# Optimization experiments

Measured on AMD Instinct MI355X. Metric: run time of the kernel, lower is better.

Reference implementation:

```python
import jax, jax.numpy as jnp
import numpy as np

B, S, D = 2, 2048, 1024
E, K, F = 8, 2, 4 * D


def setup_inputs() -> dict:
    key = jax.random.key(0)
    ks = jax.random.split(key, 5)
    sd = 1.0 / np.sqrt(D)
    sf = 1.0 / np.sqrt(F)
    x = jax.random.normal(ks[0], (B, S, D), dtype=jnp.float32)
    Wg = jax.random.uniform(ks[1], (D, E), dtype=jnp.float32, minval=-sd, maxval=sd)
    W1 = jax.random.uniform(ks[2], (E, D, F), dtype=jnp.float32, minval=-sd, maxval=sd)
    W3 = jax.random.uniform(ks[3], (D, E * F), dtype=jnp.float32, minval=-sd, maxval=sd).reshape(D, E, F).transpose(1, 0, 2)
    W2 = jax.random.uniform(ks[4], (E, F, D), dtype=jnp.float32, minval=-sf, maxval=sf)
    return {"x": x, "Wg": Wg, "W1": W1, "W2": W2, "W3": W3}


def reference(x, Wg, W1, W2, W3):
    Bx, Sx, Dx = x.shape
    xf = x.reshape(-1, Dx)  # [T, D]
    T = xf.shape[0]
    gate_logits = xf @ Wg  # [T, E]
    probs = jax.nn.softmax(gate_logits, axis=-1)
    weights, sel = jax.lax.top_k(probs, K)  # [T, K]
    weights = weights / jnp.sum(weights, axis=-1, keepdims=True)
    # scatter top-k weights into a dense [T, E] combine matrix (top-k indices are distinct)
    coef = jnp.zeros((T, W1.shape[0]), dtype=xf.dtype)
    coef = coef.at[jnp.arange(T)[:, None], sel].add(weights)
    out = jnp.zeros_like(xf)
    for e in range(W1.shape[0]):  # small fixed expert count
        h = jax.nn.silu(xf @ W1[e]) * (xf @ W3[e])  # [T, F]
        out = out + coef[:, e:e + 1] * (h @ W2[e])
    aux_loss = jnp.mean(jnp.var(gate_logits, axis=-1, ddof=1))  # torch .var() is unbiased
    return out.reshape(Bx, Sx, Dx), aux_loss
```

## Files before the change

### kernel.cpp

```cpp
#include <hip/hip_runtime.h>

typedef __bf16 bf16x8 __attribute__((ext_vector_type(8)));
typedef float  f32x4  __attribute__((ext_vector_type(4)));

#define TOKS 4096
#define DIM  1024
#define NEXP 8
#define NF   4096
#define CAP  4096
#define BM 128
#define BN 128
#define BK 64

typedef __attribute__((address_space(3))) unsigned int as3_u32;
typedef __attribute__((address_space(1))) unsigned int as1_u32;
__device__ __forceinline__ void gl16(const unsigned short* g, unsigned short* l) {
  __builtin_amdgcn_global_load_lds((as1_u32*)(unsigned long long)g, (as3_u32*)l, 16, 0, 0);
}

__device__ __forceinline__ unsigned short f2bf(float f) {
  unsigned int u = __float_as_uint(f);
  u += 0x7FFFu + ((u >> 16) & 1u);
  return (unsigned short)(u >> 16);
}
__device__ __forceinline__ int swzo(int major) {
  return ((major & 7) ^ ((major >> 3) & 7)) << 3;
}
__device__ __forceinline__ int swz8(int row, int chunk) {
  return (chunk ^ (row & 7)) << 3;
}

__global__ void moe_route(const float* __restrict__ x, const float* __restrict__ Wg,
                          int* __restrict__ pairCnt, int* __restrict__ pairIdx,
                          float* __restrict__ pairWgt, float* __restrict__ auxSum)
{
  int lane = threadIdx.x & 63;
  int tok  = blockIdx.x * 4 + (threadIdx.x >> 6);
  const float* xr = x + (size_t)tok * DIM;
  float acc[8];
  #pragma unroll
  for (int e = 0; e < 8; ++e) acc[e] = 0.f;
  #pragma unroll
  for (int i = 0; i < 16; ++i) {
    int d = i * 64 + lane;
    float xv = xr[d];
    const float4* wr = (const float4*)(Wg + d * 8);
    float4 wa = wr[0], wb = wr[1];
    acc[0] += xv * wa.x; acc[1] += xv * wa.y; acc[2] += xv * wa.z; acc[3] += xv * wa.w;
    acc[4] += xv * wb.x; acc[5] += xv * wb.y; acc[6] += xv * wb.z; acc[7] += xv * wb.w;
  }
  #pragma unroll
  for (int e = 0; e < 8; ++e) {
    float v = acc[e];
    #pragma unroll
    for (int off = 32; off; off >>= 1) v += __shfl_xor(v, off);
    acc[e] = v;
  }
  if (lane == 0) {
    int e1 = 0; float l1 = acc[0];
    #pragma unroll
    for (int e = 1; e < 8; ++e) if (acc[e] > l1) { l1 = acc[e]; e1 = e; }
    int e2 = -1; float l2 = -3.4e38f;
    #pragma unroll
    for (int e = 0; e < 8; ++e) if (e != e1 && acc[e] > l2) { l2 = acc[e]; e2 = e; }
    float r  = expf(l2 - l1);
    float w1 = 1.f / (1.f + r);
    float w2 = r / (1.f + r);
    int s1 = atomicAdd(&pairCnt[e1], 1);
    pairIdx[e1 * CAP + s1] = tok * 2;     pairWgt[e1 * CAP + s1] = w1;
    int s2 = atomicAdd(&pairCnt[e2], 1);
    pairIdx[e2 * CAP + s2] = tok * 2 + 1; pairWgt[e2 * CAP + s2] = w2;
    float m = 0.f;
    #pragma unroll
    for (int e = 0; e < 8; ++e) m += acc[e];
    m *= 0.125f;
    float v = 0.f;
    #pragma unroll
    for (int e = 0; e < 8; ++e) { float dd = acc[e] - m; v += dd * dd; }
    atomicAdd(auxSum, v * (1.f / 7.f));
  }
}

__global__ void moe_aux_final(const float* __restrict__ auxSum, float* __restrict__ outScalar) {
  *outScalar = auxSum[0] * (1.f / (float)TOKS);
}

__global__ __launch_bounds__(256) void cvt_x(const float* __restrict__ in,
                                             unsigned short* __restrict__ o)
{
  int i = (blockIdx.x * 256 + threadIdx.x) * 16;
  const float4* s = (const float4*)(in + i);
  float4 a = s[0], b = s[1], c = s[2], d = s[3];
  union { unsigned short u[8]; uint4 q; } p0, p1;
  p0.u[0]=f2bf(a.x); p0.u[1]=f2bf(a.y); p0.u[2]=f2bf(a.z); p0.u[3]=f2bf(a.w);
  p0.u[4]=f2bf(b.x); p0.u[5]=f2bf(b.y); p0.u[6]=f2bf(b.z); p0.u[7]=f2bf(b.w);
  p1.u[0]=f2bf(c.x); p1.u[1]=f2bf(c.y); p1.u[2]=f2bf(c.z); p1.u[3]=f2bf(c.w);
  p1.u[4]=f2bf(d.x); p1.u[5]=f2bf(d.y); p1.u[6]=f2bf(d.z); p1.u[7]=f2bf(d.w);
  *(uint4*)(o + i)     = p0.q;
  *(uint4*)(o + i + 8) = p1.q;
}

__global__ __launch_bounds__(256) void cvt_transpose(
    const float* __restrict__ in, unsigned short* __restrict__ outp, int R, int C)
{
  __shared__ unsigned short tile[64 * 72];
  int e  = blockIdx.z;
  int r0 = blockIdx.x * 64, c0 = blockIdx.y * 64;
  const float*    ine  = in   + (size_t)e * R * C;
  unsigned short* oute = outp + (size_t)e * R * C;
  int t = threadIdx.x;
  int r = t >> 2, cs = (t & 3) * 16;
  const float4* src = (const float4*)(ine + (size_t)(r0 + r) * C + c0 + cs);
  #pragma unroll
  for (int j = 0; j < 4; ++j) {
    float4 v = src[j];
    tile[(cs + j * 4 + 0) * 72 + r] = f2bf(v.x);
    tile[(cs + j * 4 + 1) * 72 + r] = f2bf(v.y);
    tile[(cs + j * 4 + 2) * 72 + r] = f2bf(v.z);
    tile[(cs + j * 4 + 3) * 72 + r] = f2bf(v.w);
  }
  __syncthreads();
  int c = t >> 2, rs = (t & 3) * 16;
  uint4 o0 = *(const uint4*)&tile[c * 72 + rs];
  uint4 o1 = *(const uint4*)&tile[c * 72 + rs + 8];
  unsigned short* dst = oute + (size_t)(c0 + c) * R + r0 + rs;
  *(uint4*)dst       = o0;
  *(uint4*)(dst + 8) = o1;
}

__global__ __launch_bounds__(512) void moe_ffn1_g(
    const unsigned short* __restrict__ xbf, const unsigned short* __restrict__ W1T,
    const unsigned short* __restrict__ W3T,
    const int* __restrict__ pairCnt, const int* __restrict__ pairIdx,
    unsigned short* __restrict__ hbuf)
{
  int bid = blockIdx.x;
  int m_t = (bid >> 3) & 31;
  int n_t = (bid & 7) | (((bid >> 8) & 3) << 3);
  int e   = bid >> 10;
  int cnt = pairCnt[e];
  int m0  = m_t * BM;
  if (m0 >= cnt) return;
  int n0  = n_t * BN;
  __shared__ __attribute__((aligned(16))) unsigned short As[BM * BK];
  __shared__ __attribute__((aligned(16))) unsigned short B1s[BN * BK];
  __shared__ __attribute__((aligned(16))) unsigned short B3s[BN * BK];
  __shared__ int rowPid[BM];
  int tid = threadIdx.x, lane = tid & 63, wid = tid >> 6;
  if (tid < BM) {
    int gi = m0 + tid;
    rowPid[tid] = (gi < cnt) ? pairIdx[e * CAP + gi] : -1;
  }
  const unsigned short* W1e = W1T + (size_t)e * NF * DIM + (size_t)n0 * DIM;
  const unsigned short* W3e = W3T + (size_t)e * NF * DIM + (size_t)n0 * DIM;
  f32x4 zero = {0.f, 0.f, 0.f, 0.f};
  f32x4 acc1[2][4], acc2[2][4];
  #pragma unroll
  for (int mi = 0; mi < 2; ++mi)
    #pragma unroll
    for (int ni = 0; ni < 4; ++ni) { acc1[mi][ni] = zero; acc2[mi][ni] = zero; }
  int wm = (wid >> 1) * 32, wn = (wid & 1) * 64;
  __syncthreads();

  int r0a = wid * 16 + (lane >> 3), r1a = r0a + 8;
  int p0 = rowPid[r0a], p1 = rowPid[r1a];
  size_t tk0 = (size_t)((p0 >= 0) ? (p0 >> 1) : 0);
  size_t tk1 = (size_t)((p1 >= 0) ? (p1 >> 1) : 0);
  int ch0 = ((lane & 7) ^ (r0a & 7)) * 8;
  int ch1 = ((lane & 7) ^ (r1a & 7)) * 8;
  const unsigned short* gA0  = xbf + tk0 * DIM + ch0;
  const unsigned short* gA1  = xbf + tk1 * DIM + ch1;
  const unsigned short* gB10 = W1e + (size_t)r0a * DIM + ch0;
  const unsigned short* gB11 = W1e + (size_t)r1a * DIM + ch1;
  const unsigned short* gB30 = W3e + (size_t)r0a * DIM + ch0;
  const unsigned short* gB31 = W3e + (size_t)r1a * DIM + ch1;
  unsigned short* lA0  = &As [(wid * 16) * BK];
  unsigned short* lA1  = &As [(wid * 16 + 8) * BK];
  unsigned short* lB10 = &B1s[(wid * 16) * BK];
  unsigned short* lB11 = &B1s[(wid * 16 + 8) * BK];
  unsigned short* lB30 = &B3s[(wid * 16) * BK];
  unsigned short* lB31 = &B3s[(wid * 16 + 8) * BK];

  for (int kt = 0; kt < DIM; kt += BK) {
    gl16(gA0 + kt, lA0);  gl16(gA1 + kt, lA1);
    gl16(gB10 + kt, lB10); gl16(gB11 + kt, lB11);
    gl16(gB30 + kt, lB30); gl16(gB31 + kt, lB31);
    __syncthreads();
    #pragma unroll
    for (int ks = 0; ks < 2; ++ks) {
      int kc = ks * 4 + (lane >> 4);
      bf16x8 af[2];
      #pragma unroll
      for (int mi = 0; mi < 2; ++mi) {
        int row = wm + mi * 16 + (lane & 15);
        af[mi] = *(const bf16x8*)(&As[row * BK + swz8(row, kc)]);
      }
      #pragma unroll
      for (int ni = 0; ni < 4; ++ni) {
        int f = wn + ni * 16 + (lane & 15);
        bf16x8 b1 = *(const bf16x8*)(&B1s[f * BK + swz8(f, kc)]);
        bf16x8 b3 = *(const bf16x8*)(&B3s[f * BK + swz8(f, kc)]);
        #pragma unroll
        for (int mi = 0; mi < 2; ++mi) {
          acc1[mi][ni] = __builtin_amdgcn_mfma_f32_16x16x32_bf16(af[mi], b1, acc1[mi][ni], 0, 0, 0);
          acc2[mi][ni] = __builtin_amdgcn_mfma_f32_16x16x32_bf16(af[mi], b3, acc2[mi][ni], 0, 0, 0);
        }
      }
    }
    __syncthreads();
  }
  #pragma unroll
  for (int mi = 0; mi < 2; ++mi) {
    #pragma unroll
    for (int r = 0; r < 4; ++r) {
      int row = wm + mi * 16 + ((lane >> 4) << 2) + r;
      int pid = rowPid[row];
      if (pid < 0) continue;
      size_t hb = (size_t)pid * NF + n0 + wn + (lane & 15);
      #pragma unroll
      for (int ni = 0; ni < 4; ++ni) {
        float a = acc1[mi][ni][r];
        float g = acc2[mi][ni][r];
        float s = 1.f / (1.f + __expf(-a));
        hbuf[hb + ni * 16] = f2bf(a * s * g);
      }
    }
  }
}

__global__ __launch_bounds__(512) void moe_ffn2_g(
    const unsigned short* __restrict__ hbuf, const unsigned short* __restrict__ W2T,
    const int* __restrict__ pairCnt, const int* __restrict__ pairIdx,
    const float* __restrict__ pairWgt, float* __restrict__ out)
{
  int bid = blockIdx.x;
  int n_t = bid & 7;
  int m_t = (bid >> 3) & 31;
  int e   = bid >> 8;
  int cnt = pairCnt[e];
  int m0  = m_t * BM;
  if (m0 >= cnt) return;
  int n0  = n_t * BN;
  __shared__ __attribute__((aligned(16))) unsigned short As[BM * BK];
  __shared__ __attribute__((aligned(16))) unsigned short Bs[BN * BK];
  __shared__ int   rowPid[BM];
  __shared__ float rowW[BM];
  int tid = threadIdx.x, lane = tid & 63, wid = tid >> 6;
  if (tid < BM) {
    int gi = m0 + tid;
    if (gi < cnt) { rowPid[tid] = pairIdx[e * CAP + gi]; rowW[tid] = pairWgt[e * CAP + gi]; }
    else          { rowPid[tid] = -1;                    rowW[tid] = 0.f; }
  }
  const unsigned short* W2e = W2T + (size_t)e * DIM * NF + (size_t)n0 * NF;
  f32x4 zero = {0.f, 0.f, 0.f, 0.f};
  f32x4 acc[2][4];
  #pragma unroll
  for (int mi = 0; mi < 2; ++mi)
    #pragma unroll
    for (int ni = 0; ni < 4; ++ni) acc[mi][ni] = zero;
  int wm = (wid >> 1) * 32, wn = (wid & 1) * 64;
  __syncthreads();

  int r0a = wid * 16 + (lane >> 3), r1a = r0a + 8;
  int p0 = rowPid[r0a], p1 = rowPid[r1a];
  size_t h0 = (size_t)((p0 >= 0) ? p0 : 0);
  size_t h1 = (size_t)((p1 >= 0) ? p1 : 0);
  int ch0 = ((lane & 7) ^ (r0a & 7)) * 8;
  int ch1 = ((lane & 7) ^ (r1a & 7)) * 8;
  const unsigned short* gA0 = hbuf + h0 * NF + ch0;
  const unsigned short* gA1 = hbuf + h1 * NF + ch1;
  const unsigned short* gB0 = W2e + (size_t)r0a * NF + ch0;
  const unsigned short* gB1 = W2e + (size_t)r1a * NF + ch1;
  unsigned short* lA0 = &As[(wid * 16) * BK];
  unsigned short* lA1 = &As[(wid * 16 + 8) * BK];
  unsigned short* lB0 = &Bs[(wid * 16) * BK];
  unsigned short* lB1 = &Bs[(wid * 16 + 8) * BK];

  for (int kt = 0; kt < NF; kt += BK) {
    gl16(gA0 + kt, lA0); gl16(gA1 + kt, lA1);
    gl16(gB0 + kt, lB0); gl16(gB1 + kt, lB1);
    __syncthreads();
    #pragma unroll
    for (int ks = 0; ks < 2; ++ks) {
      int kc = ks * 4 + (lane >> 4);
      bf16x8 af[2];
      #pragma unroll
      for (int mi = 0; mi < 2; ++mi) {
        int row = wm + mi * 16 + (lane & 15);
        af[mi] = *(const bf16x8*)(&As[row * BK + swz8(row, kc)]);
      }
      #pragma unroll
      for (int ni = 0; ni < 4; ++ni) {
        int dc = wn + ni * 16 + (lane & 15);
        bf16x8 b = *(const bf16x8*)(&Bs[dc * BK + swz8(dc, kc)]);
        #pragma unroll
        for (int mi = 0; mi < 2; ++mi)
          acc[mi][ni] = __builtin_amdgcn_mfma_f32_16x16x32_bf16(af[mi], b, acc[mi][ni], 0, 0, 0);
      }
    }
    __syncthreads();
  }
  #pragma unroll
  for (int mi = 0; mi < 2; ++mi) {
    #pragma unroll
    for (int r = 0; r < 4; ++r) {
      int row = wm + mi * 16 + ((lane >> 4) << 2) + r;
      int pid = rowPid[row];
      if (pid < 0) continue;
      float w = rowW[row];
      float* op = out + (size_t)(pid >> 1) * DIM + n0 + wn + (lane & 15);
      #pragma unroll
      for (int ni = 0; ni < 4; ++ni)
        atomicAdd(op + ni * 16, w * acc[mi][ni][r]);
    }
  }
}

__global__ __launch_bounds__(512) void moe_ffn1(
    const float* __restrict__ x, const float* __restrict__ W1, const float* __restrict__ W3,
    const int* __restrict__ pairCnt, const int* __restrict__ pairIdx,
    unsigned short* __restrict__ hbuf)
{
  int e   = blockIdx.z;
  int cnt = pairCnt[e];
  int m0  = blockIdx.x * BM;
  if (m0 >= cnt) return;
  int n0  = blockIdx.y * BN;
  __shared__ __attribute__((aligned(16))) unsigned short As[BM * BK];
  __shared__ __attribute__((aligned(16))) unsigned short B1s[BN * BK];
  __shared__ __attribute__((aligned(16))) unsigned short B3s[BN * BK];
  __shared__ int rowPid[BM];
  int tid = threadIdx.x;
  if (tid < BM) {
    int gi = m0 + tid;
    rowPid[tid] = (gi < cnt) ? pairIdx[e * CAP + gi] : -1;
  }
  const float* W1e = W1 + (size_t)e * DIM * NF;
  const float* W3e = W3 + (size_t)e * DIM * NF;
  f32x4 zero = {0.f, 0.f, 0.f, 0.f};
  f32x4 acc1[2][4], acc2[2][4];
  #pragma unroll
  for (int mi = 0; mi < 2; ++mi)
    #pragma unroll
    for (int ni = 0; ni < 4; ++ni) { acc1[mi][ni] = zero; acc2[mi][ni] = zero; }
  int lane = tid & 63, wid = tid >> 6;
  int wm = (wid >> 1) * 32, wn = (wid & 1) * 64;

  for (int kt = 0; kt < DIM; kt += BK) {
    __syncthreads();
    #pragma unroll
    for (int it = 0; it < 4; ++it) {
      int row = it * 32 + (tid >> 4);
      int dq  = tid & 15;
      int pid = rowPid[row];
      int tk  = (pid >= 0) ? (pid >> 1) : 0;
      float4 v = *(const float4*)(x + (size_t)tk * DIM + kt + dq * 4);
      ushort4 b; b.x = f2bf(v.x); b.y = f2bf(v.y); b.z = f2bf(v.z); b.w = f2bf(v.w);
      *(ushort4*)(&As[row * BK + ((dq * 4) ^ swzo(row))]) = b;
    }
    #pragma unroll
    for (int it = 0; it < 4; ++it) {
      int d  = it * 16 + (tid >> 5);
      int fq = tid & 31;
      size_t go = (size_t)(kt + d) * NF + n0 + fq * 4;
      float4 v1 = *(const float4*)(W1e + go);
      float4 v3 = *(const float4*)(W3e + go);
      const float* p1 = (const float*)&v1;
      const float* p3 = (const float*)&v3;
      #pragma unroll
      for (int i = 0; i < 4; ++i) {
        int f   = fq * 4 + i;
        int idx = f * BK + (d ^ swzo(f));
        B1s[idx] = f2bf(p1[i]);
        B3s[idx] = f2bf(p3[i]);
      }
    }
    __syncthreads();
    #pragma unroll
    for (int ks = 0; ks < 2; ++ks) {
      int kb = ks * 32 + ((lane >> 4) << 3);
      bf16x8 af[2];
      #pragma unroll
      for (int mi = 0; mi < 2; ++mi) {
        int row = wm + mi * 16 + (lane & 15);
        af[mi] = *(const bf16x8*)(&As[row * BK + (kb ^ swzo(row))]);
      }
      #pragma unroll
      for (int ni = 0; ni < 4; ++ni) {
        int f = wn + ni * 16 + (lane & 15);
        bf16x8 b1 = *(const bf16x8*)(&B1s[f * BK + (kb ^ swzo(f))]);
        bf16x8 b3 = *(const bf16x8*)(&B3s[f * BK + (kb ^ swzo(f))]);
        #pragma unroll
        for (int mi = 0; mi < 2; ++mi) {
          acc1[mi][ni] = __builtin_amdgcn_mfma_f32_16x16x32_bf16(af[mi], b1, acc1[mi][ni], 0, 0, 0);
          acc2[mi][ni] = __builtin_amdgcn_mfma_f32_16x16x32_bf16(af[mi], b3, acc2[mi][ni], 0, 0, 0);
        }
      }
    }
  }
  #pragma unroll
  for (int mi = 0; mi < 2; ++mi) {
    #pragma unroll
    for (int r = 0; r < 4; ++r) {
      int row = wm + mi * 16 + ((lane >> 4) << 2) + r;
      int pid = rowPid[row];
      if (pid < 0) continue;
      size_t hb = (size_t)pid * NF + n0 + wn + (lane & 15);
      #pragma unroll
      for (int ni = 0; ni < 4; ++ni) {
        float a = acc1[mi][ni][r];
        float g = acc2[mi][ni][r];
        float s = 1.f / (1.f + __expf(-a));
        hbuf[hb + ni * 16] = f2bf(a * s * g);
      }
    }
  }
}

__global__ __launch_bounds__(512) void moe_ffn2(
    const unsigned short* __restrict__ hbuf, const float* __restrict__ W2,
    const int* __restrict__ pairCnt, const int* __restrict__ pairIdx,
    const float* __restrict__ pairWgt, float* __restrict__ out)
{
  int e   = blockIdx.z;
  int cnt = pairCnt[e];
  int m0  = blockIdx.x * BM;
  if (m0 >= cnt) return;
  int n0  = blockIdx.y * BN;
  __shared__ __attribute__((aligned(16))) unsigned short As[BM * BK];
  __shared__ __attribute__((aligned(16))) unsigned short Bs[BN * BK];
  __shared__ int   rowPid[BM];
  __shared__ float rowW[BM];
  int tid = threadIdx.x;
  if (tid < BM) {
    int gi = m0 + tid;
    if (gi < cnt) { rowPid[tid] = pairIdx[e * CAP + gi]; rowW[tid] = pairWgt[e * CAP + gi]; }
    else          { rowPid[tid] = -1;                    rowW[tid] = 0.f; }
  }
  const float* W2e = W2 + (size_t)e * NF * DIM;
  f32x4 zero = {0.f, 0.f, 0.f, 0.f};
  f32x4 acc[2][4];
  #pragma unroll
  for (int mi = 0; mi < 2; ++mi)
    #pragma unroll
    for (int ni = 0; ni < 4; ++ni) acc[mi][ni] = zero;
  int lane = tid & 63, wid = tid >> 6;
  int wm = (wid >> 1) * 32, wn = (wid & 1) * 64;

  for (int kt = 0; kt < NF; kt += BK) {
    __syncthreads();
    #pragma unroll
    for (int it = 0; it < 2; ++it) {
      int row = it * 64 + (tid >> 3);
      int c8  = tid & 7;
      int pid = rowPid[row];
      int pr  = (pid >= 0) ? pid : 0;
      uint4 v = *(const uint4*)(hbuf + (size_t)pr * NF + kt + c8 * 8);
      *(uint4*)(&As[row * BK + ((c8 * 8) ^ swzo(row))]) = v;
    }
    #pragma unroll
    for (int it = 0; it < 4; ++it) {
      int fk = it * 16 + (tid >> 5);
      int dq = tid & 31;
      float4 v = *(const float4*)(W2e + (size_t)(kt + fk) * DIM + n0 + dq * 4);
      const float* p = (const float*)&v;
      #pragma unroll
      for (int i = 0; i < 4; ++i) {
        int dc = dq * 4 + i;
        Bs[dc * BK + (fk ^ swzo(dc))] = f2bf(p[i]);
      }
    }
    __syncthreads();
    #pragma unroll
    for (int ks = 0; ks < 2; ++ks) {
      int kb = ks * 32 + ((lane >> 4) << 3);
      bf16x8 af[2];
      #pragma unroll
      for (int mi = 0; mi < 2; ++mi) {
        int row = wm + mi * 16 + (lane & 15);
        af[mi] = *(const bf16x8*)(&As[row * BK + (kb ^ swzo(row))]);
      }
      #pragma unroll
      for (int ni = 0; ni < 4; ++ni) {
        int dc = wn + ni * 16 + (lane & 15);
        bf16x8 b = *(const bf16x8*)(&Bs[dc * BK + (kb ^ swzo(dc))]);
        #pragma unroll
        for (int mi = 0; mi < 2; ++mi)
          acc[mi][ni] = __builtin_amdgcn_mfma_f32_16x16x32_bf16(af[mi], b, acc[mi][ni], 0, 0, 0);
      }
    }
  }
  #pragma unroll
  for (int mi = 0; mi < 2; ++mi) {
    #pragma unroll
    for (int r = 0; r < 4; ++r) {
      int row = wm + mi * 16 + ((lane >> 4) << 2) + r;
      int pid = rowPid[row];
      if (pid < 0) continue;
      float w = rowW[row];
      float* op = out + (size_t)(pid >> 1) * DIM + n0 + wn + (lane & 15);
      #pragma unroll
      for (int ni = 0; ni < 4; ++ni)
        atomicAdd(op + ni * 16, w * acc[mi][ni][r]);
    }
  }
}

extern "C" void kernel_launch(void* const* d_in, const int* in_sizes, int n_in,
                              void* d_out, int out_size, void* d_ws, size_t ws_size,
                              hipStream_t stream)
{
  const float* x  = (const float*)d_in[0];
  const float* Wg = (const float*)d_in[1];
  const float* W1 = (const float*)d_in[2];
  const float* W2 = (const float*)d_in[3];
  const float* W3 = (const float*)d_in[4];
  float* out = (float*)d_out;
  char*  ws  = (char*)d_ws;
  int*   pairCnt = (int*)ws;
  float* auxSum  = (float*)(ws + 64);
  int*   pairIdx = (int*)(ws + 4096);
  float* pairWgt = (float*)(ws + 262144);
  unsigned short* xbf  = (unsigned short*)(ws + ((size_t)1 << 20));
  unsigned short* hbuf = (unsigned short*)(ws + ((size_t)9 << 20));
  unsigned short* W1T  = (unsigned short*)(ws + ((size_t)73 << 20));
  unsigned short* W3T  = (unsigned short*)(ws + ((size_t)137 << 20));
  unsigned short* W2T  = (unsigned short*)(ws + ((size_t)201 << 20));
  const size_t WS_NEED = (size_t)265 << 20;

  hipMemsetAsync(ws, 0, 128, stream);
  hipMemsetAsync(d_out, 0, (size_t)out_size * sizeof(float), stream);
  moe_route<<<TOKS / 4, 256, 0, stream>>>(x, Wg, pairCnt, pairIdx, pairWgt, auxSum);
  moe_aux_final<<<1, 1, 0, stream>>>(auxSum, out + (out_size - 1));

  if (ws_size >= WS_NEED) {
    cvt_x<<<TOKS * DIM / (256 * 16), 256, 0, stream>>>(x, xbf);
    cvt_transpose<<<dim3(DIM / 64, NF / 64, NEXP), 256, 0, stream>>>(W1, W1T, DIM, NF);
    cvt_transpose<<<dim3(DIM / 64, NF / 64, NEXP), 256, 0, stream>>>(W3, W3T, DIM, NF);
    cvt_transpose<<<dim3(NF / 64, DIM / 64, NEXP), 256, 0, stream>>>(W2, W2T, NF, DIM);
    moe_ffn1_g<<<(TOKS / BM) * (NF / BN) * NEXP, 512, 0, stream>>>(xbf, W1T, W3T, pairCnt, pairIdx, hbuf);
    moe_ffn2_g<<<(TOKS / BM) * (DIM / BN) * NEXP, 512, 0, stream>>>(hbuf, W2T, pairCnt, pairIdx, pairWgt, out);
  } else {
    moe_ffn1<<<dim3(TOKS / BM, NF / BN, NEXP), 512, 0, stream>>>(x, W1, W3, pairCnt, pairIdx, hbuf);
    moe_ffn2<<<dim3(TOKS / BM, DIM / BN, NEXP), 512, 0, stream>>>(hbuf, W2, pairCnt, pairIdx, pairWgt, out);
  }
}
```

Before: 545.1 us.

## Double-buffer LDS tiles in MoE FFN GEMMs and load A fragments directly to registers

Both grouped expert GEMMs now keep two LDS buffers and issue the next K-tile's global-to-LDS loads before computing on the current one, using an explicit vmcnt drain plus barrier. This overlaps memory latency with MFMA work instead of serialising load, sync and compute. In FFN1 the gathered token rows of x are loaded straight into registers per lane rather than staged through LDS, which frees shared memory for the second weight buffer. The trade-offs are more LDS per block, a full vmcnt(0) drain at every barrier, and uncoalesced register gathers for the A operand.

```diff
diff --git a/kernel.cpp b/kernel.cpp
--- a/kernel.cpp
+++ b/kernel.cpp
@@ -17,6 +17,10 @@
 __device__ __forceinline__ void gl16(const unsigned short* g, unsigned short* l) {
   __builtin_amdgcn_global_load_lds((as1_u32*)(unsigned long long)g, (as3_u32*)l, 16, 0, 0);
 }
+#define DRAIN_BAR() do { \
+  asm volatile("s_waitcnt vmcnt(0)" ::: "memory"); \
+  __builtin_amdgcn_s_barrier(); \
+} while (0)
 
 __device__ __forceinline__ unsigned short f2bf(float f) {
   unsigned int u = __float_as_uint(f);
@@ -128,7 +132,24 @@
   *(uint4*)(dst + 8) = o1;
 }
 
-__global__ __launch_bounds__(512) void moe_ffn1_g(
+__device__ __forceinline__ void ffn1_mma(
+    const unsigned short* B1b, const unsigned short* B3b,
+    bf16x8 a0, bf16x8 a1, int kc, int wn, int lane,
+    f32x4 acc1[2][4], f32x4 acc2[2][4])
+{
+  #pragma unroll
+  for (int ni = 0; ni < 4; ++ni) {
+    int f = wn + ni * 16 + (lane & 15);
+    bf16x8 b1 = *(const bf16x8*)(&B1b[f * BK + swz8(f, kc)]);
+    bf16x8 b3 = *(const bf16x8*)(&B3b[f * BK + swz8(f, kc)]);
+    acc1[0][ni] = __builtin_amdgcn_mfma_f32_16x16x32_bf16(a0, b1, acc1[0][ni], 0, 0, 0);
+    acc2[0][ni] = __builtin_amdgcn_mfma_f32_16x16x32_bf16(a0, b3, acc2[0][ni], 0, 0, 0);
+    acc1[1][ni] = __builtin_amdgcn_mfma_f32_16x16x32_bf16(a1, b1, acc1[1][ni], 0, 0, 0);
+    acc2[1][ni] = __builtin_amdgcn_mfma_f32_16x16x32_bf16(a1, b3, acc2[1][ni], 0, 0, 0);
+  }
+}
+
+__global__ __launch_bounds__(512, 4) void moe_ffn1_p(
     const unsigned short* __restrict__ xbf, const unsigned short* __restrict__ W1T,
     const unsigned short* __restrict__ W3T,
     const int* __restrict__ pairCnt, const int* __restrict__ pairIdx,
@@ -142,9 +163,8 @@
   int m0  = m_t * BM;
   if (m0 >= cnt) return;
   int n0  = n_t * BN;
-  __shared__ __attribute__((aligned(16))) unsigned short As[BM * BK];
-  __shared__ __attribute__((aligned(16))) unsigned short B1s[BN * BK];
-  __shared__ __attribute__((aligned(16))) unsigned short B3s[BN * BK];
+  __shared__ __attribute__((aligned(16))) unsigned short B1s[2][BN * BK];
+  __shared__ __attribute__((aligned(16))) unsigned short B3s[2][BN * BK];
   __shared__ int rowPid[BM];
   int tid = threadIdx.x, lane = tid & 63, wid = tid >> 6;
   if (tid < BM) {
@@ -163,51 +183,53 @@
   __syncthreads();
 
   int r0a = wid * 16 + (lane >> 3), r1a = r0a + 8;
-  int p0 = rowPid[r0a], p1 = rowPid[r1a];
-  size_t tk0 = (size_t)((p0 >= 0) ? (p0 >> 1) : 0);
-  size_t tk1 = (size_t)((p1 >= 0) ? (p1 >> 1) : 0);
   int ch0 = ((lane & 7) ^ (r0a & 7)) * 8;
   int ch1 = ((lane & 7) ^ (r1a & 7)) * 8;
-  const unsigned short* gA0  = xbf + tk0 * DIM + ch0;
-  const unsigned short* gA1  = xbf + tk1 * DIM + ch1;
   const unsigned short* gB10 = W1e + (size_t)r0a * DIM + ch0;
   const unsigned short* gB11 = W1e + (size_t)r1a * DIM + ch1;
   const unsigned short* gB30 = W3e + (size_t)r0a * DIM + ch0;
   const unsigned short* gB31 = W3e + (size_t)r1a * DIM + ch1;
-  unsigned short* lA0  = &As [(wid * 16) * BK];
-  unsigned short* lA1  = &As [(wid * 16 + 8) * BK];
-  unsigned short* lB10 = &B1s[(wid * 16) * BK];
-  unsigned short* lB11 = &B1s[(wid * 16 + 8) * BK];
-  unsigned short* lB30 = &B3s[(wid * 16) * BK];
-  unsigned short* lB31 = &B3s[(wid * 16 + 8) * BK];
-
-  for (int kt = 0; kt < DIM; kt += BK) {
-    gl16(gA0 + kt, lA0);  gl16(gA1 + kt, lA1);
-    gl16(gB10 + kt, lB10); gl16(gB11 + kt, lB11);
-    gl16(gB30 + kt, lB30); gl16(gB31 + kt, lB31);
-    __syncthreads();
-    #pragma unroll
-    for (int ks = 0; ks < 2; ++ks) {
-      int kc = ks * 4 + (lane >> 4);
-      bf16x8 af[2];
-      #pragma unroll
-      for (int mi = 0; mi < 2; ++mi) {
-        int row = wm + mi * 16 + (lane & 15);
-        af[mi] = *(const bf16x8*)(&As[row * BK + swz8(row, kc)]);
-      }
-      #pragma unroll
-      for (int ni = 0; ni < 4; ++ni) {
-        int f = wn + ni * 16 + (lane & 15);
-        bf16x8 b1 = *(const bf16x8*)(&B1s[f * BK + swz8(f, kc)]);
-        bf16x8 b3 = *(const bf16x8*)(&B3s[f * BK + swz8(f, kc)]);
-        #pragma unroll
-        for (int mi = 0; mi < 2; ++mi) {
-          acc1[mi][ni] = __builtin_amdgcn_mfma_f32_16x16x32_bf16(af[mi], b1, acc1[mi][ni], 0, 0, 0);
-          acc2[mi][ni] = __builtin_amdgcn_mfma_f32_16x16x32_bf16(af[mi], b3, acc2[mi][ni], 0, 0, 0);
-        }
-      }
-    }
-    __syncthreads();
+  unsigned short* l1b0 = &B1s[0][(wid * 16) * BK];
+  unsigned short* l1b1 = &B1s[1][(wid * 16) * BK];
+  unsigned short* l3b0 = &B3s[0][(wid * 16) * BK];
+  unsigned short* l3b1 = &B3s[1][(wid * 16) * BK];
+
+  int pm0 = rowPid[wm + (lane & 15)];
+  int pm1 = rowPid[wm + 16 + (lane & 15)];
+  const unsigned short* pA0 = xbf + (size_t)((pm0 >= 0) ? (pm0 >> 1) : 0) * DIM + (lane >> 4) * 8;
+  const unsigned short* pA1 = xbf + (size_t)((pm1 >= 0) ? (pm1 >> 1) : 0) * DIM + (lane >> 4) * 8;
+
+  gl16(gB10, l1b0); gl16(gB11, l1b0 + 8 * BK);
+  gl16(gB30, l3b0); gl16(gB31, l3b0 + 8 * BK);
+  bf16x8 aA00 = *(const bf16x8*)(pA0);
+  bf16x8 aA01 = *(const bf16x8*)(pA0 + 32);
+  bf16x8 aA10 = *(const bf16x8*)(pA1);
+  bf16x8 aA11 = *(const bf16x8*)(pA1 + 32);
+  DRAIN_BAR();
+
+  for (int kt = 0; kt < DIM; kt += 2 * BK) {
+    int kN = kt + BK;
+    gl16(gB10 + kN, l1b1); gl16(gB11 + kN, l1b1 + 8 * BK);
+    gl16(gB30 + kN, l3b1); gl16(gB31 + kN, l3b1 + 8 * BK);
+    bf16x8 aB00 = *(const bf16x8*)(pA0 + kN);
+    bf16x8 aB01 = *(const bf16x8*)(pA0 + kN + 32);
+    bf16x8 aB10 = *(const bf16x8*)(pA1 + kN);
+    bf16x8 aB11 = *(const bf16x8*)(pA1 + kN + 32);
+    ffn1_mma(B1s[0], B3s[0], aA00, aA10, (lane >> 4),     wn, lane, acc1, acc2);
+    ffn1_mma(B1s[0], B3s[0], aA01, aA11, 4 + (lane >> 4), wn, lane, acc1, acc2);
+    DRAIN_BAR();
+    int kP = kt + 2 * BK;
+    if (kP < DIM) {
+      gl16(gB10 + kP, l1b0); gl16(gB11 + kP, l1b0 + 8 * BK);
+      gl16(gB30 + kP, l3b0); gl16(gB31 + kP, l3b0 + 8 * BK);
+      aA00 = *(const bf16x8*)(pA0 + kP);
+      aA01 = *(const bf16x8*)(pA0 + kP + 32);
+      aA10 = *(const bf16x8*)(pA1 + kP);
+      aA11 = *(const bf16x8*)(pA1 + kP + 32);
+    }
+    ffn1_mma(B1s[1], B3s[1], aB00, aB10, (lane >> 4),     wn, lane, acc1, acc2);
+    ffn1_mma(B1s[1], B3s[1], aB01, aB11, 4 + (lane >> 4), wn, lane, acc1, acc2);
+    DRAIN_BAR();
   }
   #pragma unroll
   for (int mi = 0; mi < 2; ++mi) {
@@ -228,7 +250,31 @@
   }
 }
 
-__global__ __launch_bounds__(512) void moe_ffn2_g(
+__device__ __forceinline__ void ffn2_mma(
+    const unsigned short* Ab, const unsigned short* Bb,
+    int wm, int wn, int lane, f32x4 acc[2][4])
+{
+  #pragma unroll
+  for (int ks = 0; ks < 2; ++ks) {
+    int kc = ks * 4 + (lane >> 4);
+    bf16x8 af[2];
+    #pragma unroll
+    for (int mi = 0; mi < 2; ++mi) {
+      int row = wm + mi * 16 + (lane & 15);
+      af[mi] = *(const bf16x8*)(&Ab[row * BK + swz8(row, kc)]);
+    }
+    #pragma unroll
+    for (int ni = 0; ni < 4; ++ni) {
+      int dc = wn + ni * 16 + (lane & 15);
+      bf16x8 b = *(const bf16x8*)(&Bb[dc * BK + swz8(dc, kc)]);
+      #pragma unroll
+      for (int mi = 0; mi < 2; ++mi)
+        acc[mi][ni] = __builtin_amdgcn_mfma_f32_16x16x32_bf16(af[mi], b, acc[mi][ni], 0, 0, 0);
+    }
+  }
+}
+
+__global__ __launch_bounds__(512, 4) void moe_ffn2_p(
     const unsigned short* __restrict__ hbuf, const unsigned short* __restrict__ W2T,
     const int* __restrict__ pairCnt, const int* __restrict__ pairIdx,
     const float* __restrict__ pairWgt, float* __restrict__ out)
@@ -241,8 +287,8 @@
   int m0  = m_t * BM;
   if (m0 >= cnt) return;
   int n0  = n_t * BN;
-  __shared__ __attribute__((aligned(16))) unsigned short As[BM * BK];
-  __shared__ __attribute__((aligned(16))) unsigned short Bs[BN * BK];
+  __shared__ __attribute__((aligned(16))) unsigned short As[2][BM * BK];
+  __shared__ __attribute__((aligned(16))) unsigned short Bs[2][BN * BK];
   __shared__ int   rowPid[BM];
   __shared__ float rowW[BM];
   int tid = threadIdx.x, lane = tid & 63, wid = tid >> 6;
@@ -271,34 +317,28 @@
   const unsigned short* gA1 = hbuf + h1 * NF + ch1;
   const unsigned short* gB0 = W2e + (size_t)r0a * NF + ch0;
   const unsigned short* gB1 = W2e + (size_t)r1a * NF + ch1;
-  unsigned short* lA0 = &As[(wid * 16) * BK];
-  unsigned short* lA1 = &As[(wid * 16 + 8) * BK];
-  unsigned short* lB0 = &Bs[(wid * 16) * BK];
-  unsigned short* lB1 = &Bs[(wid * 16 + 8) * BK];
-
-  for (int kt = 0; kt < NF; kt += BK) {
-    gl16(gA0 + kt, lA0); gl16(gA1 + kt, lA1);
-    gl16(gB0 + kt, lB0); gl16(gB1 + kt, lB1);
-    __syncthreads();
-    #pragma unroll
-    for (int ks = 0; ks < 2; ++ks) {
-      int kc = ks * 4 + (lane >> 4);
-      bf16x8 af[2];
-      #pragma unroll
-      for (int mi = 0; mi < 2; ++mi) {
-        int row = wm + mi * 16 + (lane & 15);
-        af[mi] = *(const bf16x8*)(&As[row * BK + swz8(row, kc)]);
-      }
-      #pragma unroll
-      for (int ni = 0; ni < 4; ++ni) {
-        int dc = wn + ni * 16 + (lane & 15);
-        bf16x8 b = *(const bf16x8*)(&Bs[dc * BK + swz8(dc, kc)]);
-        #pragma unroll
-        for (int mi = 0; mi < 2; ++mi)
-          acc[mi][ni] = __builtin_amdgcn_mfma_f32_16x16x32_bf16(af[mi], b, acc[mi][ni], 0, 0, 0);
-      }
-    }
-    __syncthreads();
+  unsigned short* lab0 = &As[0][(wid * 16) * BK];
+  unsigned short* lab1 = &As[1][(wid * 16) * BK];
+  unsigned short* lbb0 = &Bs[0][(wid * 16) * BK];
+  unsigned short* lbb1 = &Bs[1][(wid * 16) * BK];
+
+  gl16(gA0, lab0); gl16(gA1, lab0 + 8 * BK);
+  gl16(gB0, lbb0); gl16(gB1, lbb0 + 8 * BK);
+  DRAIN_BAR();
+
+  for (int kt = 0; kt < NF; kt += 2 * BK) {
+    int kN = kt + BK;
+    gl16(gA0 + kN, lab1); gl16(gA1 + kN, lab1 + 8 * BK);
+    gl16(gB0 + kN, lbb1); gl16(gB1 + kN, lbb1 + 8 * BK);
+    ffn2_mma(As[0], Bs[0], wm, wn, lane, acc);
+    DRAIN_BAR();
+    int kP = kt + 2 * BK;
+    if (kP < NF) {
+      gl16(gA0 + kP, lab0); gl16(gA1 + kP, lab0 + 8 * BK);
+      gl16(gB0 + kP, lbb0); gl16(gB1 + kP, lbb0 + 8 * BK);
+    }
+    ffn2_mma(As[1], Bs[1], wm, wn, lane, acc);
+    DRAIN_BAR();
   }
   #pragma unroll
   for (int mi = 0; mi < 2; ++mi) {
@@ -538,8 +578,8 @@
     cvt_transpose<<<dim3(DIM / 64, NF / 64, NEXP), 256, 0, stream>>>(W1, W1T, DIM, NF);
     cvt_transpose<<<dim3(DIM / 64, NF / 64, NEXP), 256, 0, stream>>>(W3, W3T, DIM, NF);
     cvt_transpose<<<dim3(NF / 64, DIM / 64, NEXP), 256, 0, stream>>>(W2, W2T, NF, DIM);
-    moe_ffn1_g<<<(TOKS / BM) * (NF / BN) * NEXP, 512, 0, stream>>>(xbf, W1T, W3T, pairCnt, pairIdx, hbuf);
-    moe_ffn2_g<<<(TOKS / BM) * (DIM / BN) * NEXP, 512, 0, stream>>>(hbuf, W2T, pairCnt, pairIdx, pairWgt, out);
+    moe_ffn1_p<<<(TOKS / BM) * (NF / BN) * NEXP, 512, 0, stream>>>(xbf, W1T, W3T, pairCnt, pairIdx, hbuf);
+    moe_ffn2_p<<<(TOKS / BM) * (DIM / BN) * NEXP, 512, 0, stream>>>(hbuf, W2T, pairCnt, pairIdx, pairWgt, out);
   } else {
     moe_ffn1<<<dim3(TOKS / BM, NF / BN, NEXP), 512, 0, stream>>>(x, W1, W3, pairCnt, pairIdx, hbuf);
     moe_ffn2<<<dim3(TOKS / BM, DIM / BN, NEXP), 512, 0, stream>>>(hbuf, W2, pairCnt, pairIdx, pairWgt, out);
```

Measured after the change: 734.0 us. 34.7% more time.

## Interleave W1/W3 into one transposed buffer and halve FFN1 accumulator tiles

Applied to the files above, without the earlier changes.

W1 and W3 are now converted and transposed together into one interleaved bf16 buffer, alternating 16-row groups of each. FFN1 loads a single B tile per K step and computes gate and up projections as adjacent column groups inside one accumulator set. This halves the per-block accumulator registers and shared memory, which should raise occupancy, and also fuses two conversion launches into one. In exchange FFN1 launches twice as many blocks, and each block reloads its A tile for only 64 output features.

```diff
diff --git a/kernel.cpp b/kernel.cpp
--- a/kernel.cpp
+++ b/kernel.cpp
@@ -128,37 +128,78 @@
   *(uint4*)(dst + 8) = o1;
 }
 
-__global__ __launch_bounds__(512) void moe_ffn1_g(
-    const unsigned short* __restrict__ xbf, const unsigned short* __restrict__ W1T,
-    const unsigned short* __restrict__ W3T,
+__global__ __launch_bounds__(256) void cvt_w13(
+    const float* __restrict__ W1, const float* __restrict__ W3,
+    unsigned short* __restrict__ outp)
+{
+  __shared__ unsigned short t1[64 * 72];
+  __shared__ unsigned short t3[64 * 72];
+  int e  = blockIdx.z;
+  int r0 = blockIdx.x * 64, c0 = blockIdx.y * 64;
+  const float* in1 = W1 + (size_t)e * DIM * NF;
+  const float* in3 = W3 + (size_t)e * DIM * NF;
+  unsigned short* oute = outp + (size_t)e * (2 * NF) * DIM;
+  int t = threadIdx.x;
+  int r = t >> 2, cs = (t & 3) * 16;
+  const float4* s1 = (const float4*)(in1 + (size_t)(r0 + r) * NF + c0 + cs);
+  const float4* s3 = (const float4*)(in3 + (size_t)(r0 + r) * NF + c0 + cs);
+  #pragma unroll
+  for (int j = 0; j < 4; ++j) {
+    float4 v1 = s1[j];
+    float4 v3 = s3[j];
+    int cb = cs + j * 4;
+    t1[(cb + 0) * 72 + r] = f2bf(v1.x);
+    t1[(cb + 1) * 72 + r] = f2bf(v1.y);
+    t1[(cb + 2) * 72 + r] = f2bf(v1.z);
+    t1[(cb + 3) * 72 + r] = f2bf(v1.w);
+    t3[(cb + 0) * 72 + r] = f2bf(v3.x);
+    t3[(cb + 1) * 72 + r] = f2bf(v3.y);
+    t3[(cb + 2) * 72 + r] = f2bf(v3.z);
+    t3[(cb + 3) * 72 + r] = f2bf(v3.w);
+  }
+  __syncthreads();
+  int c = t >> 2, rs = (t & 3) * 16;
+  int drow = c0 * 2 + (c >> 4) * 32 + (c & 15);
+  uint4 a0 = *(const uint4*)&t1[c * 72 + rs];
+  uint4 a1 = *(const uint4*)&t1[c * 72 + rs + 8];
+  uint4 b0 = *(const uint4*)&t3[c * 72 + rs];
+  uint4 b1 = *(const uint4*)&t3[c * 72 + rs + 8];
+  unsigned short* d1 = oute + (size_t)drow * DIM + r0 + rs;
+  unsigned short* d3 = d1 + (size_t)16 * DIM;
+  *(uint4*)d1       = a0;
+  *(uint4*)(d1 + 8) = a1;
+  *(uint4*)d3       = b0;
+  *(uint4*)(d3 + 8) = b1;
+}
+
+__global__ __launch_bounds__(512) void moe_ffn1_i(
+    const unsigned short* __restrict__ xbf, const unsigned short* __restrict__ W13T,
     const int* __restrict__ pairCnt, const int* __restrict__ pairIdx,
     unsigned short* __restrict__ hbuf)
 {
   int bid = blockIdx.x;
   int m_t = (bid >> 3) & 31;
-  int n_t = (bid & 7) | (((bid >> 8) & 3) << 3);
-  int e   = bid >> 10;
+  int n_t = (bid & 7) | (((bid >> 8) & 7) << 3);
+  int e   = bid >> 11;
   int cnt = pairCnt[e];
   int m0  = m_t * BM;
   if (m0 >= cnt) return;
-  int n0  = n_t * BN;
+  int n0f = n_t * 64;
   __shared__ __attribute__((aligned(16))) unsigned short As[BM * BK];
-  __shared__ __attribute__((aligned(16))) unsigned short B1s[BN * BK];
-  __shared__ __attribute__((aligned(16))) unsigned short B3s[BN * BK];
+  __shared__ __attribute__((aligned(16))) unsigned short Bs[BN * BK];
   __shared__ int rowPid[BM];
   int tid = threadIdx.x, lane = tid & 63, wid = tid >> 6;
   if (tid < BM) {
     int gi = m0 + tid;
     rowPid[tid] = (gi < cnt) ? pairIdx[e * CAP + gi] : -1;
   }
-  const unsigned short* W1e = W1T + (size_t)e * NF * DIM + (size_t)n0 * DIM;
-  const unsigned short* W3e = W3T + (size_t)e * NF * DIM + (size_t)n0 * DIM;
+  const unsigned short* W13e = W13T + (size_t)e * (2 * NF) * DIM + (size_t)n_t * 128 * DIM;
   f32x4 zero = {0.f, 0.f, 0.f, 0.f};
-  f32x4 acc1[2][4], acc2[2][4];
+  f32x4 acc[2][4];
   #pragma unroll
   for (int mi = 0; mi < 2; ++mi)
     #pragma unroll
-    for (int ni = 0; ni < 4; ++ni) { acc1[mi][ni] = zero; acc2[mi][ni] = zero; }
+    for (int ni = 0; ni < 4; ++ni) acc[mi][ni] = zero;
   int wm = (wid >> 1) * 32, wn = (wid & 1) * 64;
   __syncthreads();
 
@@ -168,23 +209,18 @@
   size_t tk1 = (size_t)((p1 >= 0) ? (p1 >> 1) : 0);
   int ch0 = ((lane & 7) ^ (r0a & 7)) * 8;
   int ch1 = ((lane & 7) ^ (r1a & 7)) * 8;
-  const unsigned short* gA0  = xbf + tk0 * DIM + ch0;
-  const unsigned short* gA1  = xbf + tk1 * DIM + ch1;
-  const unsigned short* gB10 = W1e + (size_t)r0a * DIM + ch0;
-  const unsigned short* gB11 = W1e + (size_t)r1a * DIM + ch1;
-  const unsigned short* gB30 = W3e + (size_t)r0a * DIM + ch0;
-  const unsigned short* gB31 = W3e + (size_t)r1a * DIM + ch1;
-  unsigned short* lA0  = &As [(wid * 16) * BK];
-  unsigned short* lA1  = &As [(wid * 16 + 8) * BK];
-  unsigned short* lB10 = &B1s[(wid * 16) * BK];
-  unsigned short* lB11 = &B1s[(wid * 16 + 8) * BK];
-  unsigned short* lB30 = &B3s[(wid * 16) * BK];
-  unsigned short* lB31 = &B3s[(wid * 16 + 8) * BK];
+  const unsigned short* gA0 = xbf + tk0 * DIM + ch0;
+  const unsigned short* gA1 = xbf + tk1 * DIM + ch1;
+  const unsigned short* gB0 = W13e + (size_t)r0a * DIM + ch0;
+  const unsigned short* gB1 = W13e + (size_t)r1a * DIM + ch1;
+  unsigned short* lA0 = &As[(wid * 16) * BK];
+  unsigned short* lA1 = &As[(wid * 16 + 8) * BK];
+  unsigned short* lB0 = &Bs[(wid * 16) * BK];
+  unsigned short* lB1 = &Bs[(wid * 16 + 8) * BK];
 
   for (int kt = 0; kt < DIM; kt += BK) {
-    gl16(gA0 + kt, lA0);  gl16(gA1 + kt, lA1);
-    gl16(gB10 + kt, lB10); gl16(gB11 + kt, lB11);
-    gl16(gB30 + kt, lB30); gl16(gB31 + kt, lB31);
+    gl16(gA0 + kt, lA0); gl16(gA1 + kt, lA1);
+    gl16(gB0 + kt, lB0); gl16(gB1 + kt, lB1);
     __syncthreads();
     #pragma unroll
     for (int ks = 0; ks < 2; ++ks) {
@@ -197,14 +233,11 @@
       }
       #pragma unroll
       for (int ni = 0; ni < 4; ++ni) {
-        int f = wn + ni * 16 + (lane & 15);
-        bf16x8 b1 = *(const bf16x8*)(&B1s[f * BK + swz8(f, kc)]);
-        bf16x8 b3 = *(const bf16x8*)(&B3s[f * BK + swz8(f, kc)]);
+        int br = wn + ni * 16 + (lane & 15);
+        bf16x8 b = *(const bf16x8*)(&Bs[br * BK + swz8(br, kc)]);
         #pragma unroll
-        for (int mi = 0; mi < 2; ++mi) {
-          acc1[mi][ni] = __builtin_amdgcn_mfma_f32_16x16x32_bf16(af[mi], b1, acc1[mi][ni], 0, 0, 0);
-          acc2[mi][ni] = __builtin_amdgcn_mfma_f32_16x16x32_bf16(af[mi], b3, acc2[mi][ni], 0, 0, 0);
-        }
+        for (int mi = 0; mi < 2; ++mi)
+          acc[mi][ni] = __builtin_amdgcn_mfma_f32_16x16x32_bf16(af[mi], b, acc[mi][ni], 0, 0, 0);
       }
     }
     __syncthreads();
@@ -216,13 +249,13 @@
       int row = wm + mi * 16 + ((lane >> 4) << 2) + r;
       int pid = rowPid[row];
       if (pid < 0) continue;
-      size_t hb = (size_t)pid * NF + n0 + wn + (lane & 15);
-      #pragma unroll
-      for (int ni = 0; ni < 4; ++ni) {
-        float a = acc1[mi][ni][r];
-        float g = acc2[mi][ni][r];
+      size_t hb = (size_t)pid * NF + n0f + (wn >> 1) + (lane & 15);
+      #pragma unroll
+      for (int fg = 0; fg < 2; ++fg) {
+        float a = acc[mi][fg * 2 + 0][r];
+        float g = acc[mi][fg * 2 + 1][r];
         float s = 1.f / (1.f + __expf(-a));
-        hbuf[hb + ni * 16] = f2bf(a * s * g);
+        hbuf[hb + fg * 16] = f2bf(a * s * g);
       }
     }
   }
@@ -523,8 +556,7 @@
   float* pairWgt = (float*)(ws + 262144);
   unsigned short* xbf  = (unsigned short*)(ws + ((size_t)1 << 20));
   unsigned short* hbuf = (unsigned short*)(ws + ((size_t)9 << 20));
-  unsigned short* W1T  = (unsigned short*)(ws + ((size_t)73 << 20));
-  unsigned short* W3T  = (unsigned short*)(ws + ((size_t)137 << 20));
+  unsigned short* W13T = (unsigned short*)(ws + ((size_t)73 << 20));
   unsigned short* W2T  = (unsigned short*)(ws + ((size_t)201 << 20));
   const size_t WS_NEED = (size_t)265 << 20;
 
@@ -535,10 +567,9 @@
 
   if (ws_size >= WS_NEED) {
     cvt_x<<<TOKS * DIM / (256 * 16), 256, 0, stream>>>(x, xbf);
-    cvt_transpose<<<dim3(DIM / 64, NF / 64, NEXP), 256, 0, stream>>>(W1, W1T, DIM, NF);
-    cvt_transpose<<<dim3(DIM / 64, NF / 64, NEXP), 256, 0, stream>>>(W3, W3T, DIM, NF);
+    cvt_w13<<<dim3(DIM / 64, NF / 64, NEXP), 256, 0, stream>>>(W1, W3, W13T);
     cvt_transpose<<<dim3(NF / 64, DIM / 64, NEXP), 256, 0, stream>>>(W2, W2T, NF, DIM);
-    moe_ffn1_g<<<(TOKS / BM) * (NF / BN) * NEXP, 512, 0, stream>>>(xbf, W1T, W3T, pairCnt, pairIdx, hbuf);
+    moe_ffn1_i<<<(TOKS / BM) * (2 * NF / BN) * NEXP, 512, 0, stream>>>(xbf, W13T, pairCnt, pairIdx, hbuf);
     moe_ffn2_g<<<(TOKS / BM) * (DIM / BN) * NEXP, 512, 0, stream>>>(hbuf, W2T, pairCnt, pairIdx, pairWgt, out);
   } else {
     moe_ffn1<<<dim3(TOKS / BM, NF / BN, NEXP), 512, 0, stream>>>(x, W1, W3, pairCnt, pairIdx, hbuf);
```

Result: no change. 546.1 us (+0.2%).
